# Performance work log

Hardware: AMD Instinct MI355X
Metric: run time of the kernel (lower is better)

The kernel has to match this reference:

```python
import jax, jax.numpy as jnp
import numpy as np

IN_FEATURES = 4096
OUT_FEATURES = 11008
BATCH = 256


def unpack_i4(q):
    # q: [K//2, N] packed bytes; row 2k = low nibble, row 2k+1 = high nibble
    low = q & 15
    high = (q >> 4) & 15
    # interleave -> [K, N]
    return jnp.stack([low, high], axis=1).reshape(q.shape[0] * 2, q.shape[1])


def setup_inputs() -> dict:
    key = jax.random.key(0)
    k1, k2, k3, k4 = jax.random.split(key, 4)
    x = jax.random.normal(k1, (BATCH, IN_FEATURES), dtype=jnp.float32)
    qweight = jax.random.randint(k2, (IN_FEATURES // 2, OUT_FEATURES), 0, 256, dtype=jnp.int32)
    scales = jax.random.uniform(k3, (OUT_FEATURES,), dtype=jnp.float32)
    zeroes = jax.random.normal(k4, (OUT_FEATURES,), dtype=jnp.float32)
    return {"x": x, "qweight": qweight, "scales": scales, "zeroes": zeroes}


def reference(x, qweight, scales, zeroes):
    # Dequantize: per-output-channel scale/zero over unpacked int4 weights
    w = scales[None, :] * unpack_i4(qweight).astype(jnp.float32) - zeroes[None, :]  # [K, N]
    return x @ w  # [B, N]
```

## Files before the change

kernel.cpp:

```cpp
#include <hip/hip_runtime.h>
#include <stdint.h>

#define K_DIM 4096
#define N_DIM 11008
#define M_DIM 256

typedef uint32_t u32;
using frag_ab = __attribute__((ext_vector_type(8))) short;
using frag_cd = __attribute__((ext_vector_type(4))) float;

typedef __attribute__((address_space(3))) const char lds_cc;

#define DSR128(dst, addr, off)                                       \
    asm volatile("ds_read_b128 %0, %1 offset:" #off                  \
                 : "=&v"(dst) : "v"(addr))
#define DSR32(dst, addr, off)                                        \
    asm volatile("ds_read_b32 %0, %1 offset:" #off                   \
                 : "=&v"(dst) : "v"(addr))

__device__ __forceinline__ u32 f2bf_rn(float f) {
    u32 u = __builtin_bit_cast(u32, f);
    return (u + 0x7FFFu + ((u >> 16) & 1u)) >> 16;
}
__device__ __forceinline__ float bf2f(u32 b) {
    return __builtin_bit_cast(float, b << 16);
}
__device__ __forceinline__ void gll16(const void* g, void* l) {
    __builtin_amdgcn_global_load_lds(
        (const __attribute__((address_space(1))) u32*)g,
        (__attribute__((address_space(3))) u32*)l, 16, 0, 0);
}

#define BFCVT(q) ((u32)((__mul24((int)(q), 0x4004) & 0x003C003C) | 0x42004200))

__global__ __launch_bounds__(256) void prep_kernel(const float* __restrict__ x,
                                                   ushort* __restrict__ xbf,
                                                   float* __restrict__ rowsum) {
    const int row = blockIdx.x;
    const int tid = threadIdx.x;
    const float* xr = x + (size_t)row * K_DIM;
    ushort* br = xbf + (size_t)row * K_DIM;
    float s = 0.0f;
#pragma unroll
    for (int p = 0; p < 4; ++p) {
        int i = p * 1024 + tid * 4;
        float4 v = *reinterpret_cast<const float4*>(xr + i);
        u32 b0 = f2bf_rn(v.x), b1 = f2bf_rn(v.y), b2 = f2bf_rn(v.z), b3 = f2bf_rn(v.w);
        uint2 o;
        o.x = b0 | (b1 << 16);
        o.y = b2 | (b3 << 16);
        *reinterpret_cast<uint2*>(br + i) = o;
        s += bf2f(b0) + bf2f(b1) + bf2f(b2) + bf2f(b3);
    }
#pragma unroll
    for (int off = 32; off > 0; off >>= 1) s += __shfl_down(s, off, 64);
    __shared__ float wsum[4];
    if ((tid & 63) == 0) wsum[tid >> 6] = s;
    __syncthreads();
    if (tid == 0) rowsum[row] = wsum[0] + wsum[1] + wsum[2] + wsum[3];
}

__global__ __launch_bounds__(512, 4) void gemm_kernel(const int* __restrict__ qw,
                                                      const float* __restrict__ scales,
                                                      const float* __restrict__ zeroes,
                                                      const ushort* __restrict__ xbf,
                                                      const float* __restrict__ rowsum,
                                                      float* __restrict__ out,
                                                      ushort* __restrict__ partial,
                                                      int split4) {
    __shared__ uint4 Alds[3][1024];
    __shared__ u32   Blds[3][2048];

    const u32* qwu = (const u32*)qw;
    const int tid  = threadIdx.x;
    const int lane = tid & 63;
    const int wid  = tid >> 6;
    const int l4   = lane & 15;
    const int c    = lane >> 4;

    const int orig = blockIdx.x;
    int nb, sp, NTt;
    if (split4) {
        int wg = (orig & 7) * 43 + (orig >> 3);
        nb = wg >> 2; sp = wg & 3; NTt = 32;
    } else {
        nb = orig; sp = 0; NTt = 128;
    }
    const int n0 = nb * 128;
    const int wm = wid >> 1;
    const int wn = wid & 1;

    const ushort* asrc[2];
#pragma unroll
    for (int j = 0; j < 2; ++j)
        asrc[j] = xbf + (size_t)(j * 128 + wid * 16 + (lane >> 2)) * K_DIM +
                  sp * 1024 + 8 * ((lane & 3) ^ ((lane >> 3) & 3));
    const u32* bsrc = qwu + (size_t)(sp * 512 + wid * 2 + (lane >> 5)) * N_DIM +
                      n0 + 4 * ((lane & 31) ^ (((wid >> 1) & 1) << 2));

    const u32 aoff  = (u32)((wm * 64 + l4) * 64 + ((c ^ ((l4 >> 1) & 3)) << 4));
    const u32 b0off = (u32)((c * 4) * 512 + (wn * 64 + ((c & 1) << 4) + l4) * 4);
    const u32 b1off = (u32)((c * 4) * 512 + (wn * 64 + ((1 ^ (c & 1)) << 4) + l4) * 4);

    frag_cd acc[4][4];
#pragma unroll
    for (int i = 0; i < 4; ++i)
#pragma unroll
        for (int j = 0; j < 4; ++j)
            acc[i][j] = (frag_cd){0.f, 0.f, 0.f, 0.f};

    auto stage = [&](int t, int buf) {
#pragma unroll
        for (int j = 0; j < 2; ++j)
            gll16(asrc[j] + (size_t)t * 32, &Alds[buf][j * 512 + wid * 64]);
        gll16(bsrc + (size_t)t * 16 * N_DIM, &Blds[buf][wid * 256]);
    };

    auto compute = [&](int buf) {
        lds_cc* Ab = (lds_cc*)&Alds[buf][0];
        lds_cc* Bb = (lds_cc*)&Blds[buf][0];
        frag_ab afr[4];
        DSR128(afr[0], Ab + aoff, 0);
        DSR128(afr[1], Ab + aoff, 1024);
        DSR128(afr[2], Ab + aoff, 2048);
        DSR128(afr[3], Ab + aoff, 3072);
        u32 bq[16];
        DSR32(bq[0],  Bb + b0off, 0);
        DSR32(bq[1],  Bb + b0off, 512);
        DSR32(bq[2],  Bb + b0off, 1024);
        DSR32(bq[3],  Bb + b0off, 1536);
        DSR32(bq[4],  Bb + b1off, 0);
        DSR32(bq[5],  Bb + b1off, 512);
        DSR32(bq[6],  Bb + b1off, 1024);
        DSR32(bq[7],  Bb + b1off, 1536);
        DSR32(bq[8],  Bb + b0off, 128);
        DSR32(bq[9],  Bb + b0off, 640);
        DSR32(bq[10], Bb + b0off, 1152);
        DSR32(bq[11], Bb + b0off, 1664);
        DSR32(bq[12], Bb + b1off, 128);
        DSR32(bq[13], Bb + b1off, 640);
        DSR32(bq[14], Bb + b1off, 1152);
        DSR32(bq[15], Bb + b1off, 1664);
        asm volatile("s_waitcnt lgkmcnt(0)" ::: "memory");
        __builtin_amdgcn_sched_barrier(0);
#pragma unroll
        for (int nf = 0; nf < 4; ++nf) {
            union { frag_ab f; u32 u[4]; } bb;
            bb.u[0] = BFCVT(bq[nf * 4 + 0]);
            bb.u[1] = BFCVT(bq[nf * 4 + 1]);
            bb.u[2] = BFCVT(bq[nf * 4 + 2]);
            bb.u[3] = BFCVT(bq[nf * 4 + 3]);
#pragma unroll
            for (int mf = 0; mf < 4; ++mf)
                acc[mf][nf] = __builtin_amdgcn_mfma_f32_16x16x32_bf16(
                    afr[mf], bb.f, acc[mf][nf], 0, 0, 0);
        }
    };

    stage(0, 0);
    stage(1, 1);

    int cur = 0;
    for (int t = 0; t < NTt; ++t) {
        int pbuf = cur + 2; if (pbuf >= 3) pbuf -= 3;
        if (t + 2 < NTt) {
            stage(t + 2, pbuf);
            asm volatile("s_waitcnt vmcnt(6)" ::: "memory");
        } else if (t + 1 < NTt) {
            asm volatile("s_waitcnt vmcnt(3)" ::: "memory");
        } else {
            asm volatile("s_waitcnt vmcnt(0)" ::: "memory");
        }
        __builtin_amdgcn_s_barrier();
        __builtin_amdgcn_sched_barrier(0);
        compute(cur);
        asm volatile("" ::: "memory");
        __builtin_amdgcn_s_barrier();
        ++cur; if (cur >= 3) cur -= 3;
    }

    float sc[4], zp[4];
#pragma unroll
    for (int nf = 0; nf < 4; ++nf) {
        int n = n0 + wn * 64 + nf * 16 + l4;
        sc[nf] = scales[n];
        zp[nf] = zeroes[n] + 32.0f * sc[nf];
    }
    if (sp == 0) {
        float rs[4][4];
#pragma unroll
        for (int mf = 0; mf < 4; ++mf)
#pragma unroll
            for (int j = 0; j < 4; ++j)
                rs[mf][j] = rowsum[wm * 64 + mf * 16 + c * 4 + j];
#pragma unroll
        for (int mf = 0; mf < 4; ++mf)
#pragma unroll
            for (int nf = 0; nf < 4; ++nf)
#pragma unroll
                for (int j = 0; j < 4; ++j) {
                    int m = wm * 64 + mf * 16 + c * 4 + j;
                    out[(size_t)m * N_DIM + n0 + wn * 64 + nf * 16 + l4] =
                        sc[nf] * acc[mf][nf][j] - zp[nf] * rs[mf][j];
                }
    } else {
        ushort* pb = partial + (size_t)(sp - 1) * M_DIM * N_DIM;
#pragma unroll
        for (int mf = 0; mf < 4; ++mf)
#pragma unroll
            for (int nf = 0; nf < 4; ++nf)
#pragma unroll
                for (int j = 0; j < 4; ++j) {
                    int m = wm * 64 + mf * 16 + c * 4 + j;
                    pb[(size_t)m * N_DIM + n0 + wn * 64 + nf * 16 + l4] =
                        (ushort)f2bf_rn(sc[nf] * acc[mf][nf][j]);
                }
    }
}

__global__ __launch_bounds__(256) void reduce_kernel(float* __restrict__ out,
                                                     const ushort* __restrict__ partial) {
    const size_t NTOT = (size_t)M_DIM * N_DIM;
    size_t i = ((size_t)blockIdx.x * 256 + threadIdx.x) * 4;
    float4 o = *reinterpret_cast<float4*>(out + i);
    ushort4 a = *reinterpret_cast<const ushort4*>(partial + i);
    ushort4 b = *reinterpret_cast<const ushort4*>(partial + NTOT + i);
    ushort4 d = *reinterpret_cast<const ushort4*>(partial + 2 * NTOT + i);
    o.x += bf2f(a.x) + bf2f(b.x) + bf2f(d.x);
    o.y += bf2f(a.y) + bf2f(b.y) + bf2f(d.y);
    o.z += bf2f(a.z) + bf2f(b.z) + bf2f(d.z);
    o.w += bf2f(a.w) + bf2f(b.w) + bf2f(d.w);
    *reinterpret_cast<float4*>(out + i) = o;
}

extern "C" void kernel_launch(void* const* d_in, const int* in_sizes, int n_in,
                              void* d_out, int out_size, void* d_ws, size_t ws_size,
                              hipStream_t stream) {
    const float* x      = (const float*)d_in[0];
    const int*   qw     = (const int*)d_in[1];
    const float* scales = (const float*)d_in[2];
    const float* zeroes = (const float*)d_in[3];
    float* out = (float*)d_out;

    const size_t XBF_BYTES = (size_t)M_DIM * K_DIM * 2;
    const size_t RS_OFF    = XBF_BYTES;
    const size_t P_OFF     = XBF_BYTES + 4096;
    const size_t P_BYTES   = (size_t)3 * M_DIM * N_DIM * 2;

    ushort* xbf    = (ushort*)d_ws;
    float*  rowsum = (float*)((char*)d_ws + RS_OFF);
    ushort* part   = (ushort*)((char*)d_ws + P_OFF);

    const bool split4 = ws_size >= P_OFF + P_BYTES;

    prep_kernel<<<M_DIM, 256, 0, stream>>>(x, xbf, rowsum);
    if (split4) {
        gemm_kernel<<<344, 512, 0, stream>>>(qw, scales, zeroes, xbf, rowsum,
                                             out, part, 1);
        reduce_kernel<<<(M_DIM * N_DIM) / (256 * 4), 256, 0, stream>>>(out, part);
    } else {
        gemm_kernel<<<86, 512, 0, stream>>>(qw, scales, zeroes, xbf, rowsum,
                                            out, nullptr, 0);
    }
}
```

Measured before the change: 53.41 us.

## Load int4 weights directly into registers, drop B LDS staging

Quantized weight tiles are now fetched with global_load_dwordx4 straight into registers, double-buffered one tile ahead, instead of being staged through LDS and read back with many ds_read_b32. The A buffer ring grows to four stages and one barrier per iteration is removed. The output column mapping is permuted so each lane owns four adjacent columns, which makes epilogue stores vectorized float4/ushort4 writes. This trades LDS traffic and barriers for more VGPRs and exposed global latency, and it relies on the column permutation lining up with the MFMA layout.

```diff
diff --git a/kernel.cpp b/kernel.cpp
--- a/kernel.cpp
+++ b/kernel.cpp
@@ -8,15 +8,14 @@
 typedef uint32_t u32;
 using frag_ab = __attribute__((ext_vector_type(8))) short;
 using frag_cd = __attribute__((ext_vector_type(4))) float;
+using u32x4   = __attribute__((ext_vector_type(4))) uint32_t;
 
 typedef __attribute__((address_space(3))) const char lds_cc;
 
 #define DSR128(dst, addr, off)                                       \
     asm volatile("ds_read_b128 %0, %1 offset:" #off                  \
                  : "=&v"(dst) : "v"(addr))
-#define DSR32(dst, addr, off)                                        \
-    asm volatile("ds_read_b32 %0, %1 offset:" #off                   \
-                 : "=&v"(dst) : "v"(addr))
+#define VMW(n) asm volatile("s_waitcnt vmcnt(" #n ")" ::: "memory")
 
 __device__ __forceinline__ u32 f2bf_rn(float f) {
     u32 u = __builtin_bit_cast(u32, f);
@@ -68,10 +67,8 @@
                                                       float* __restrict__ out,
                                                       ushort* __restrict__ partial,
                                                       int split4) {
-    __shared__ uint4 Alds[3][1024];
-    __shared__ u32   Blds[3][2048];
-
-    const u32* qwu = (const u32*)qw;
+    __shared__ uint4 Alds[4][1024];
+
     const int tid  = threadIdx.x;
     const int lane = tid & 63;
     const int wid  = tid >> 6;
@@ -95,12 +92,14 @@
     for (int j = 0; j < 2; ++j)
         asrc[j] = xbf + (size_t)(j * 128 + wid * 16 + (lane >> 2)) * K_DIM +
                   sp * 1024 + 8 * ((lane & 3) ^ ((lane >> 3) & 3));
-    const u32* bsrc = qwu + (size_t)(sp * 512 + wid * 2 + (lane >> 5)) * N_DIM +
-                      n0 + 4 * ((lane & 31) ^ (((wid >> 1) & 1) << 2));
-
-    const u32 aoff  = (u32)((wm * 64 + l4) * 64 + ((c ^ ((l4 >> 1) & 3)) << 4));
-    const u32 b0off = (u32)((c * 4) * 512 + (wn * 64 + ((c & 1) << 4) + l4) * 4);
-    const u32 b1off = (u32)((c * 4) * 512 + (wn * 64 + ((1 ^ (c & 1)) << 4) + l4) * 4);
+
+    const char* bbase = (const char*)qw + ((size_t)sp * 512 * N_DIM + n0) * 4;
+    u32 vb[4];
+#pragma unroll
+    for (int p = 0; p < 4; ++p)
+        vb[p] = (u32)(((c * 4 + p) * N_DIM + wn * 64 + 4 * l4) * 4);
+
+    const u32 aoff = (u32)((wm * 64 + l4) * 64 + ((c ^ ((l4 >> 1) & 3)) << 4));
 
     frag_cd acc[4][4];
 #pragma unroll
@@ -109,113 +108,107 @@
         for (int j = 0; j < 4; ++j)
             acc[i][j] = (frag_cd){0.f, 0.f, 0.f, 0.f};
 
-    auto stage = [&](int t, int buf) {
+    u32x4 Bq0[4], Bq1[4];
+
+#define ISSUE_B(QS, t) {                                                     \
+    const char* _b = bbase + (size_t)(t) * ((size_t)16 * N_DIM * 4);         \
+    asm volatile("global_load_dwordx4 %0, %4, %8\n\t"                        \
+                 "global_load_dwordx4 %1, %5, %8\n\t"                        \
+                 "global_load_dwordx4 %2, %6, %8\n\t"                        \
+                 "global_load_dwordx4 %3, %7, %8"                            \
+                 : "=&v"(QS[0]), "=&v"(QS[1]), "=&v"(QS[2]), "=&v"(QS[3])    \
+                 : "v"(vb[0]), "v"(vb[1]), "v"(vb[2]), "v"(vb[3]), "s"(_b)); }
+
+    auto stageA = [&](int t) {
+        int buf = t & 3;
 #pragma unroll
         for (int j = 0; j < 2; ++j)
             gll16(asrc[j] + (size_t)t * 32, &Alds[buf][j * 512 + wid * 64]);
-        gll16(bsrc + (size_t)t * 16 * N_DIM, &Blds[buf][wid * 256]);
     };
 
-    auto compute = [&](int buf) {
+    auto computeTile = [&](int buf, const u32x4* Q) {
         lds_cc* Ab = (lds_cc*)&Alds[buf][0];
-        lds_cc* Bb = (lds_cc*)&Blds[buf][0];
         frag_ab afr[4];
         DSR128(afr[0], Ab + aoff, 0);
         DSR128(afr[1], Ab + aoff, 1024);
         DSR128(afr[2], Ab + aoff, 2048);
         DSR128(afr[3], Ab + aoff, 3072);
-        u32 bq[16];
-        DSR32(bq[0],  Bb + b0off, 0);
-        DSR32(bq[1],  Bb + b0off, 512);
-        DSR32(bq[2],  Bb + b0off, 1024);
-        DSR32(bq[3],  Bb + b0off, 1536);
-        DSR32(bq[4],  Bb + b1off, 0);
-        DSR32(bq[5],  Bb + b1off, 512);
-        DSR32(bq[6],  Bb + b1off, 1024);
-        DSR32(bq[7],  Bb + b1off, 1536);
-        DSR32(bq[8],  Bb + b0off, 128);
-        DSR32(bq[9],  Bb + b0off, 640);
-        DSR32(bq[10], Bb + b0off, 1152);
-        DSR32(bq[11], Bb + b0off, 1664);
-        DSR32(bq[12], Bb + b1off, 128);
-        DSR32(bq[13], Bb + b1off, 640);
-        DSR32(bq[14], Bb + b1off, 1152);
-        DSR32(bq[15], Bb + b1off, 1664);
         asm volatile("s_waitcnt lgkmcnt(0)" ::: "memory");
         __builtin_amdgcn_sched_barrier(0);
 #pragma unroll
-        for (int nf = 0; nf < 4; ++nf) {
+        for (int j = 0; j < 4; ++j) {
             union { frag_ab f; u32 u[4]; } bb;
-            bb.u[0] = BFCVT(bq[nf * 4 + 0]);
-            bb.u[1] = BFCVT(bq[nf * 4 + 1]);
-            bb.u[2] = BFCVT(bq[nf * 4 + 2]);
-            bb.u[3] = BFCVT(bq[nf * 4 + 3]);
+            bb.u[0] = BFCVT(Q[0][j]);
+            bb.u[1] = BFCVT(Q[1][j]);
+            bb.u[2] = BFCVT(Q[2][j]);
+            bb.u[3] = BFCVT(Q[3][j]);
 #pragma unroll
             for (int mf = 0; mf < 4; ++mf)
-                acc[mf][nf] = __builtin_amdgcn_mfma_f32_16x16x32_bf16(
-                    afr[mf], bb.f, acc[mf][nf], 0, 0, 0);
+                acc[mf][j] = __builtin_amdgcn_mfma_f32_16x16x32_bf16(
+                    afr[mf], bb.f, acc[mf][j], 0, 0, 0);
         }
     };
 
-    stage(0, 0);
-    stage(1, 1);
-
-    int cur = 0;
-    for (int t = 0; t < NTt; ++t) {
-        int pbuf = cur + 2; if (pbuf >= 3) pbuf -= 3;
-        if (t + 2 < NTt) {
-            stage(t + 2, pbuf);
-            asm volatile("s_waitcnt vmcnt(6)" ::: "memory");
-        } else if (t + 1 < NTt) {
-            asm volatile("s_waitcnt vmcnt(3)" ::: "memory");
-        } else {
-            asm volatile("s_waitcnt vmcnt(0)" ::: "memory");
+#define TILE(t, Qc, Qn) {                                                    \
+    if ((t) + 1 < NTt) ISSUE_B(Qn, (t) + 1);                                 \
+    if ((t) + 2 < NTt) stageA((t) + 2);                                      \
+    if ((t) > 0 && (t) + 2 < NTt) { VMW(8); }                                \
+    else if ((t) + 1 < NTt)       { VMW(6); }                                \
+    else                          { VMW(0); }                                \
+    __builtin_amdgcn_s_barrier();                                            \
+    __builtin_amdgcn_sched_barrier(0);                                       \
+    computeTile((t) & 3, Qc); }
+
+    stageA(0);
+    stageA(1);
+    ISSUE_B(Bq0, 0);
+
+    for (int t = 0; t < NTt; t += 2) {
+        TILE(t, Bq0, Bq1);
+        TILE(t + 1, Bq1, Bq0);
+    }
+
+    const int ce = n0 + wn * 64 + 4 * l4;
+    float sc[4], zp[4];
+#pragma unroll
+    for (int j = 0; j < 4; ++j) {
+        sc[j] = scales[ce + j];
+        zp[j] = zeroes[ce + j] + 32.0f * sc[j];
+    }
+    if (sp == 0) {
+#pragma unroll
+        for (int mf = 0; mf < 4; ++mf) {
+            const float4 rs = *reinterpret_cast<const float4*>(
+                &rowsum[wm * 64 + mf * 16 + c * 4]);
+            const float rsa[4] = {rs.x, rs.y, rs.z, rs.w};
+#pragma unroll
+            for (int j4 = 0; j4 < 4; ++j4) {
+                int m = wm * 64 + mf * 16 + c * 4 + j4;
+                float4 o;
+                o.x = sc[0] * acc[mf][0][j4] - zp[0] * rsa[j4];
+                o.y = sc[1] * acc[mf][1][j4] - zp[1] * rsa[j4];
+                o.z = sc[2] * acc[mf][2][j4] - zp[2] * rsa[j4];
+                o.w = sc[3] * acc[mf][3][j4] - zp[3] * rsa[j4];
+                *reinterpret_cast<float4*>(&out[(size_t)m * N_DIM + ce]) = o;
+            }
         }
-        __builtin_amdgcn_s_barrier();
-        __builtin_amdgcn_sched_barrier(0);
-        compute(cur);
-        asm volatile("" ::: "memory");
-        __builtin_amdgcn_s_barrier();
-        ++cur; if (cur >= 3) cur -= 3;
-    }
-
-    float sc[4], zp[4];
-#pragma unroll
-    for (int nf = 0; nf < 4; ++nf) {
-        int n = n0 + wn * 64 + nf * 16 + l4;
-        sc[nf] = scales[n];
-        zp[nf] = zeroes[n] + 32.0f * sc[nf];
-    }
-    if (sp == 0) {
-        float rs[4][4];
-#pragma unroll
-        for (int mf = 0; mf < 4; ++mf)
-#pragma unroll
-            for (int j = 0; j < 4; ++j)
-                rs[mf][j] = rowsum[wm * 64 + mf * 16 + c * 4 + j];
-#pragma unroll
-        for (int mf = 0; mf < 4; ++mf)
-#pragma unroll
-            for (int nf = 0; nf < 4; ++nf)
-#pragma unroll
-                for (int j = 0; j < 4; ++j) {
-                    int m = wm * 64 + mf * 16 + c * 4 + j;
-                    out[(size_t)m * N_DIM + n0 + wn * 64 + nf * 16 + l4] =
-                        sc[nf] * acc[mf][nf][j] - zp[nf] * rs[mf][j];
-                }
     } else {
         ushort* pb = partial + (size_t)(sp - 1) * M_DIM * N_DIM;
 #pragma unroll
         for (int mf = 0; mf < 4; ++mf)
 #pragma unroll
-            for (int nf = 0; nf < 4; ++nf)
-#pragma unroll
-                for (int j = 0; j < 4; ++j) {
-                    int m = wm * 64 + mf * 16 + c * 4 + j;
-                    pb[(size_t)m * N_DIM + n0 + wn * 64 + nf * 16 + l4] =
-                        (ushort)f2bf_rn(sc[nf] * acc[mf][nf][j]);
-                }
-    }
+            for (int j4 = 0; j4 < 4; ++j4) {
+                int m = wm * 64 + mf * 16 + c * 4 + j4;
+                ushort4 o;
+                o.x = (ushort)f2bf_rn(sc[0] * acc[mf][0][j4]);
+                o.y = (ushort)f2bf_rn(sc[1] * acc[mf][1][j4]);
+                o.z = (ushort)f2bf_rn(sc[2] * acc[mf][2][j4]);
+                o.w = (ushort)f2bf_rn(sc[3] * acc[mf][3][j4]);
+                *reinterpret_cast<ushort4*>(&pb[(size_t)m * N_DIM + ce]) = o;
+            }
+    }
+#undef TILE
+#undef ISSUE_B
 }
 
 __global__ __launch_bounds__(256) void reduce_kernel(float* __restrict__ out,
```

Measured after the change: 66.44 us. +24.4%, slower.
